# Optimization experiments

Hardware: AMD Instinct MI355X
Metric: run time of the kernel (lower is better)

## Reference

```python
import jax, jax.numpy as jnp
import numpy as np

N, DEG, F_IN, HID, OUT = 20000, 16, 128, 128, 64
E = N * DEG


def setup_inputs() -> dict:
    key = jax.random.key(0)
    ks = jax.random.split(key, 12)
    s = 0.05  # small init scale to keep activations stable
    x = jax.random.normal(ks[0], (N, F_IN), jnp.float32)
    # PyG LSTM aggregation requires edges sorted by destination; fixed degree DEG
    src = jax.random.randint(ks[1], (E,), 0, N, dtype=jnp.int32)
    dst = jnp.repeat(jnp.arange(N, dtype=jnp.int32), DEG)
    edge_index = jnp.stack([src, dst])  # [2, E]
    return {
        "x": x,
        "edge_index": edge_index,
        "lstm_Wih": jax.random.normal(ks[2], (4, 4 * HID, F_IN), jnp.float32) * s,
        "lstm_Whh": jax.random.normal(ks[3], (4, 4 * HID, HID), jnp.float32) * s,
        "lstm_bih": jax.random.normal(ks[4], (4, 4 * HID), jnp.float32) * s,
        "lstm_bhh": jax.random.normal(ks[5], (4, 4 * HID), jnp.float32) * s,
        "linl_W123": jax.random.normal(ks[6], (3, HID, HID), jnp.float32) * s,
        "linl_b123": jax.random.normal(ks[7], (3, HID), jnp.float32) * s,
        "linr_W123": jax.random.normal(ks[8], (3, HID, HID), jnp.float32) * s,
        "linl_W4": jax.random.normal(ks[9], (OUT, HID), jnp.float32) * s,
        "linl_b4": jax.random.normal(ks[10], (OUT,), jnp.float32) * s,
        "linr_W4": jax.random.normal(ks[11], (OUT, HID), jnp.float32) * s,
    }


def _lstm_last(msgs, Wih, Whh, bih, bhh):
    """Run an LSTM over the padded neighbor sequence, return h at last step.
    msgs: [n, deg, f]. Matches PyG LSTMAggregation (lstm(x)[0][:, -1])."""
    n = msgs.shape[0]
    H = Whh.shape[1]
    b = bih + bhh  # torch LSTM adds both biases

    def step(carry, xt):  # xt: [n, f]
        h, c = carry
        g = xt @ Wih.T + h @ Whh.T + b  # [n, 4H], gate order i,f,g,o
        i, f, gg, o = jnp.split(g, 4, axis=-1)
        c = jax.nn.sigmoid(f) * c + jax.nn.sigmoid(i) * jnp.tanh(gg)
        h = jax.nn.sigmoid(o) * jnp.tanh(c)
        return (h, c), None

    h0 = jnp.zeros((n, H), msgs.dtype)
    (h, _), _ = jax.lax.scan(step, (h0, h0), jnp.swapaxes(msgs, 0, 1))
    return h


def _sage_conv(x, src, Wih, Whh, bih, bhh, Wl, bl, Wr):
    """SAGEConv(aggr='lstm'): lin_l(lstm_agg(x_j)) + lin_r(x).
    Fixed degree + dst-sorted edges => to_dense_batch is a reshape."""
    n, f = x.shape
    msgs = x[src].reshape(n, DEG, f)  # gather neighbor (source) features
    agg = _lstm_last(msgs, Wih, Whh, bih, bhh)
    return agg @ Wl.T + bl + x @ Wr.T  # lin_r has no bias in PyG


def reference(x, edge_index, lstm_Wih, lstm_Whh, lstm_bih, lstm_bhh,
              linl_W123, linl_b123, linr_W123, linl_W4, linl_b4, linr_W4):
    src = edge_index[0]
    # eval mode: dropout is identity
    x1 = jax.nn.relu(_sage_conv(x, src, lstm_Wih[0], lstm_Whh[0], lstm_bih[0],
                                lstm_bhh[0], linl_W123[0], linl_b123[0], linr_W123[0]))
    x2 = jax.nn.relu(_sage_conv(x1, src, lstm_Wih[1], lstm_Whh[1], lstm_bih[1],
                                lstm_bhh[1], linl_W123[1], linl_b123[1], linr_W123[1]) + x1)
    x3 = jax.nn.relu(_sage_conv(x2, src, lstm_Wih[2], lstm_Whh[2], lstm_bih[2],
                                lstm_bhh[2], linl_W123[2], linl_b123[2], linr_W123[2]) + x2)
    x4 = _sage_conv(x3, src, lstm_Wih[3], lstm_Whh[3], lstm_bih[3], lstm_bhh[3],
                    linl_W4, linl_b4, linr_W4)
    return x4
```

## Files before the change

kernel.cpp:

```cpp
#include <hip/hip_runtime.h>


#define N_NODES 20000
#define DEG 16

typedef __bf16 bf16x8 __attribute__((ext_vector_type(8)));
typedef float f32x4 __attribute__((ext_vector_type(4)));

__device__ inline unsigned short f2bf(float f) {
  unsigned u = __builtin_bit_cast(unsigned, f);
  u += 0x7fffu + ((u >> 16) & 1u);
  return (unsigned short)(u >> 16);
}
__device__ inline float fexp2(float x) {
#if __has_builtin(__builtin_amdgcn_exp2f)
  return __builtin_amdgcn_exp2f(x);
#else
  return exp2f(x);
#endif
}
__device__ inline float frcp(float x) {
#if __has_builtin(__builtin_amdgcn_rcpf)
  return __builtin_amdgcn_rcpf(x);
#else
  return 1.f / x;
#endif
}
__device__ inline float sigm(float x) { return frcp(1.f + fexp2(-1.44269504f * x)); }
__device__ inline float tanh_(float x) { return frcp(1.f + fexp2(-2.88539008f * x)) * 2.f - 1.f; }

__device__ inline void barrier_lds() {
  asm volatile("s_waitcnt lgkmcnt(0)\n\ts_barrier" ::: "memory");
}

__global__ __launch_bounds__(256) void prep_weights(
    const float* __restrict__ Wih, const float* __restrict__ Whh,
    const float* __restrict__ bih, const float* __restrict__ bhh,
    unsigned short* __restrict__ WihB, unsigned short* __restrict__ WhhB,
    float* __restrict__ bsum) {
  int tid = blockIdx.x * 256 + threadIdx.x;
  float4 a = *(const float4*)(Wih + tid * 4);
  ushort4 o;
  o.x = f2bf(a.x); o.y = f2bf(a.y); o.z = f2bf(a.z); o.w = f2bf(a.w);
  *(ushort4*)(WihB + tid * 4) = o;
  float4 b = *(const float4*)(Whh + tid * 4);
  ushort4 p;
  p.x = f2bf(b.x); p.y = f2bf(b.y); p.z = f2bf(b.z); p.w = f2bf(b.w);
  *(ushort4*)(WhhB + tid * 4) = p;
  if (tid < 2048) bsum[tid] = bih[tid] + bhh[tid];
}

__global__ __launch_bounds__(256) void cast_bf(
    const float* __restrict__ x, unsigned short* __restrict__ xb) {
  int tid = blockIdx.x * 256 + threadIdx.x;
  float4 v = *(const float4*)(x + tid * 4);
  ushort4 o;
  o.x = f2bf(v.x); o.y = f2bf(v.y); o.z = f2bf(v.z); o.w = f2bf(v.w);
  *(ushort4*)(xb + tid * 4) = o;
}

__global__ __launch_bounds__(512, 2) void lstm_fused(
    const unsigned short* __restrict__ xbf,
    const int* __restrict__ src,
    const unsigned short* __restrict__ WihB,
    const unsigned short* __restrict__ WhhB,
    const float* __restrict__ bsum,
    float* __restrict__ agg) {
  __shared__ __align__(16) unsigned char xsb[2][32 * 256];
  __shared__ __align__(16) unsigned char hbuf[2][32 * 256];
  __shared__ __align__(16) int idx_s[512];
  const int tid = threadIdx.x;
  const int lane = tid & 63, w = tid >> 6;
  const int l15 = lane & 15, l4 = lane >> 4;
  const int node0 = blockIdx.x * 32;
  const int colb = w * 16 + l15;

  idx_s[(tid & 15) * 32 + (tid >> 4)] = src[node0 * DEG + tid];

  bf16x8 bwx[4][4], bwh[4][4];
  float bs[4];
#pragma unroll
  for (int g = 0; g < 4; ++g) {
#pragma unroll
    for (int kt = 0; kt < 4; ++kt) {
      bwx[g][kt] = *(const bf16x8*)(WihB + (g * 128 + colb) * 128 + kt * 32 + l4 * 8);
      bwh[g][kt] = *(const bf16x8*)(WhhB + (g * 128 + colb) * 128 + kt * 32 + l4 * 8);
    }
    bs[g] = bsum[g * 128 + colb];
  }
  barrier_lds();

  const int erow = w * 4 + l4;
  const int schunk = l15 ^ (erow & 7);

  {
    int idx = idx_s[erow];
    uint4 v = *(const uint4*)(xbf + idx * 128 + schunk * 8);
    *(uint4*)(&xsb[0][erow * 256 + l15 * 16]) = v;
  }
  barrier_lds();

  float c[2][4] = {{0.f, 0.f, 0.f, 0.f}, {0.f, 0.f, 0.f, 0.f}};

  for (int t = 0; t < 16; ++t) {
    uint4 xstg;
    if (t < 15) {
      int idx = idx_s[(t + 1) * 32 + erow];
      xstg = *(const uint4*)(xbf + idx * 128 + schunk * 8);
    }

    const unsigned char* xrb = xsb[t & 1];
    f32x4 acc[2][4];
#pragma unroll
    for (int rt = 0; rt < 2; ++rt)
#pragma unroll
      for (int g = 0; g < 4; ++g) acc[rt][g] = (f32x4){bs[g], bs[g], bs[g], bs[g]};

#pragma unroll
    for (int rt = 0; rt < 2; ++rt) {
      bf16x8 afx[4];
#pragma unroll
      for (int kt = 0; kt < 4; ++kt) {
        int m = rt * 16 + l15;
        int byte = (m * 256 + kt * 64 + l4 * 16) ^ ((m & 7) << 4);
        afx[kt] = *(const bf16x8*)(xrb + byte);
      }
#pragma unroll
      for (int g = 0; g < 4; ++g)
#pragma unroll
        for (int kt = 0; kt < 4; ++kt)
          acc[rt][g] = __builtin_amdgcn_mfma_f32_16x16x32_bf16(afx[kt], bwx[g][kt],
                                                               acc[rt][g], 0, 0, 0);
    }

    if (t > 0) {
      const unsigned char* hb = hbuf[(t - 1) & 1];
#pragma unroll
      for (int rt = 0; rt < 2; ++rt) {
        bf16x8 afh[4];
#pragma unroll
        for (int kt = 0; kt < 4; ++kt) {
          int m = rt * 16 + l15;
          int byte = (m * 256 + kt * 64 + l4 * 16) ^ ((m & 7) << 4);
          afh[kt] = *(const bf16x8*)(hb + byte);
        }
#pragma unroll
        for (int g = 0; g < 4; ++g)
#pragma unroll
          for (int kt = 0; kt < 4; ++kt)
            acc[rt][g] = __builtin_amdgcn_mfma_f32_16x16x32_bf16(afh[kt], bwh[g][kt],
                                                                 acc[rt][g], 0, 0, 0);
      }
    }

    float hn[2][4];
#pragma unroll
    for (int rt = 0; rt < 2; ++rt)
#pragma unroll
      for (int r = 0; r < 4; ++r) {
        float ig = sigm(acc[rt][0][r]), fg = sigm(acc[rt][1][r]);
        float gg = tanh_(acc[rt][2][r]), og = sigm(acc[rt][3][r]);
        float cn = fg * c[rt][r] + ig * gg;
        c[rt][r] = cn;
        hn[rt][r] = og * tanh_(cn);
      }

    if (t < 15) {
      unsigned char* hw = hbuf[t & 1];
#pragma unroll
      for (int rt = 0; rt < 2; ++rt)
#pragma unroll
        for (int r = 0; r < 4; ++r) {
          int m = rt * 16 + l4 * 4 + r;
          int byte = (m * 256 + colb * 2) ^ ((m & 7) << 4);
          *(__bf16*)(hw + byte) = (__bf16)hn[rt][r];
        }
      *(uint4*)(&xsb[(t + 1) & 1][erow * 256 + l15 * 16]) = xstg;
      barrier_lds();
    } else {
#pragma unroll
      for (int rt = 0; rt < 2; ++rt)
#pragma unroll
        for (int r = 0; r < 4; ++r)
          agg[(node0 + rt * 16 + l4 * 4 + r) * 128 + colb] = hn[rt][r];
    }
  }
}

__global__ __launch_bounds__(256) void gemm_out(
    const float* __restrict__ A1,
    const float* __restrict__ A2,
    const float* __restrict__ Wl, const float* __restrict__ bl,
    const float* __restrict__ Wr,
    const float* __restrict__ resid,
    float* __restrict__ out,
    unsigned short* __restrict__ outbf,
    int NOUT, int do_relu, int Nrows) {
  __shared__ __align__(16) unsigned char As[64 * 512];
  const int tid = threadIdx.x;
  const int lane = tid & 63, w = tid >> 6;
  const int l15 = lane & 15, l4 = lane >> 4;
  const int row0 = blockIdx.x * 64;

#pragma unroll
  for (int i = 0; i < 16; ++i) {
    int flat = i * 1024 + tid * 4;
    int r = flat >> 8, c = flat & 255;
    int grow = row0 + r;
    float4 v;
    if (grow < Nrows)
      v = (c < 128) ? *(const float4*)(A1 + grow * 128 + c)
                    : *(const float4*)(A2 + grow * 128 + (c - 128));
    else
      v = make_float4(0.f, 0.f, 0.f, 0.f);
    ushort4 b;
    b.x = f2bf(v.x); b.y = f2bf(v.y); b.z = f2bf(v.z); b.w = f2bf(v.w);
    int byte = (r * 512 + c * 2) ^ ((r & 7) << 4);
    *(ushort4*)(As + byte) = b;
  }
  __syncthreads();

  const int colg = blockIdx.y * 64 + w * 16 + l15;
  bf16x8 bw[8];
#pragma unroll
  for (int kt = 0; kt < 8; ++kt) {
    const float* bp = (kt < 4) ? (Wl + colg * 128 + kt * 32 + l4 * 8)
                               : (Wr + colg * 128 + (kt - 4) * 32 + l4 * 8);
    float4 a = *(const float4*)bp;
    float4 b = *(const float4*)(bp + 4);
    bf16x8 v;
    v[0] = (__bf16)a.x; v[1] = (__bf16)a.y; v[2] = (__bf16)a.z; v[3] = (__bf16)a.w;
    v[4] = (__bf16)b.x; v[5] = (__bf16)b.y; v[6] = (__bf16)b.z; v[7] = (__bf16)b.w;
    bw[kt] = v;
  }

  f32x4 acc[4];
#pragma unroll
  for (int rt = 0; rt < 4; ++rt) acc[rt] = (f32x4){0.f, 0.f, 0.f, 0.f};

#pragma unroll
  for (int kt = 0; kt < 8; ++kt) {
#pragma unroll
    for (int rt = 0; rt < 4; ++rt) {
      int m = rt * 16 + l15;
      int byte = (m * 512 + kt * 64 + l4 * 16) ^ ((m & 7) << 4);
      bf16x8 af = *(const bf16x8*)(As + byte);
      acc[rt] = __builtin_amdgcn_mfma_f32_16x16x32_bf16(af, bw[kt], acc[rt], 0, 0, 0);
    }
  }

  const float bias = bl[colg];
#pragma unroll
  for (int rt = 0; rt < 4; ++rt)
#pragma unroll
    for (int r = 0; r < 4; ++r) {
      int grow = row0 + rt * 16 + l4 * 4 + r;
      if (grow < Nrows) {
        float v = acc[rt][r] + bias;
        if (resid) v += resid[grow * 128 + colg];
        if (do_relu) v = fmaxf(v, 0.f);
        out[grow * NOUT + colg] = v;
        if (outbf) outbf[grow * 128 + colg] = f2bf(v);
      }
    }
}

extern "C" void kernel_launch(void* const* d_in, const int* in_sizes, int n_in,
                              void* d_out, int out_size, void* d_ws, size_t ws_size,
                              hipStream_t stream) {
  const float* X = (const float*)d_in[0];
  const int* src = (const int*)d_in[1];
  const float* Wih = (const float*)d_in[2];
  const float* Whh = (const float*)d_in[3];
  const float* bih = (const float*)d_in[4];
  const float* bhh = (const float*)d_in[5];
  const float* Wl123 = (const float*)d_in[6];
  const float* bl123 = (const float*)d_in[7];
  const float* Wr123 = (const float*)d_in[8];
  const float* Wl4 = (const float*)d_in[9];
  const float* bl4 = (const float*)d_in[10];
  const float* Wr4 = (const float*)d_in[11];
  float* out = (float*)d_out;

  char* ws = (char*)d_ws;
  unsigned short* xbf = (unsigned short*)ws;
  float* agg = (float*)(ws + 5120000);
  float* xb0 = (float*)(ws + 15360000);
  float* xb1 = (float*)(ws + 25600000);
  unsigned short* WihB = (unsigned short*)(ws + 35840000);
  unsigned short* WhhB = (unsigned short*)(ws + 36364288);
  float* bsumW = (float*)(ws + 36888576);

  prep_weights<<<dim3(256), 256, 0, stream>>>(Wih, Whh, bih, bhh, WihB, WhhB, bsumW);
  cast_bf<<<dim3(2500), 256, 0, stream>>>(X, xbf);

  const float* xcur = X;
  for (int L = 0; L < 4; ++L) {
    lstm_fused<<<dim3(625), 512, 0, stream>>>(xbf, src, WihB + L * 65536,
                                              WhhB + L * 65536, bsumW + L * 512, agg);
    if (L < 3) {
      float* nxt = (L & 1) ? xb1 : xb0;
      gemm_out<<<dim3(313, 2), 256, 0, stream>>>(agg, xcur, Wl123 + L * 16384,
                                                 bl123 + L * 128, Wr123 + L * 16384,
                                                 (L >= 1) ? xcur : nullptr, nxt, xbf,
                                                 128, 1, N_NODES);
      xcur = nxt;
    } else {
      gemm_out<<<dim3(313, 1), 256, 0, stream>>>(agg, xcur, Wl4, bl4, Wr4, nullptr, out,
                                                 nullptr, 64, 0, N_NODES);
    }
  }
}
```

Baseline: 546.0 us.

## Process 80 nodes per LSTM block and interleave per-row-tile gate compute

Each LSTM block now handles 80 nodes (5 row tiles) instead of 32, so the per-block weight register load is amortized over more nodes and the grid drops from 625 to 250 blocks. The loop is restructured so each row tile runs its x and h MFMAs, gate math and h store in sequence, which keeps only one tile's accumulators live and lets activation math overlap with the next tile's MFMAs. Gather staging grows to three uint4 loads per thread. The risks are that 250 blocks leaves many of the MI355X's CUs underused, and that the larger LDS footprint may reduce occupancy.

```diff
diff --git a/kernel.cpp b/kernel.cpp
--- a/kernel.cpp
+++ b/kernel.cpp
@@ -3,6 +3,8 @@
 
 #define N_NODES 20000
 #define DEG 16
+#define NPB 80
+#define RT 5
 
 typedef __bf16 bf16x8 __attribute__((ext_vector_type(8)));
 typedef float f32x4 __attribute__((ext_vector_type(4)));
@@ -66,16 +68,23 @@
     const unsigned short* __restrict__ WhhB,
     const float* __restrict__ bsum,
     float* __restrict__ agg) {
-  __shared__ __align__(16) unsigned char xsb[2][32 * 256];
-  __shared__ __align__(16) unsigned char hbuf[2][32 * 256];
-  __shared__ __align__(16) int idx_s[512];
+  __shared__ __align__(16) unsigned char xsb[2][NPB * 256];
+  __shared__ __align__(16) unsigned char hbuf[2][NPB * 256];
+  __shared__ __align__(16) int idx_s[NPB * DEG];
   const int tid = threadIdx.x;
   const int lane = tid & 63, w = tid >> 6;
   const int l15 = lane & 15, l4 = lane >> 4;
-  const int node0 = blockIdx.x * 32;
+  const int node0 = blockIdx.x * NPB;
   const int colb = w * 16 + l15;
 
-  idx_s[(tid & 15) * 32 + (tid >> 4)] = src[node0 * DEG + tid];
+#pragma unroll
+  for (int i = 0; i < 3; ++i) {
+    int task = tid + i * 512;
+    if (task < NPB * DEG) {
+      int node = task >> 4, t = task & 15;
+      idx_s[t * NPB + node] = src[node0 * DEG + task];
+    }
+  }
 
   bf16x8 bwx[4][4], bwh[4][4];
   float bs[4];
@@ -90,99 +99,95 @@
   }
   barrier_lds();
 
-  const int erow = w * 4 + l4;
-  const int schunk = l15 ^ (erow & 7);
+  const int task0 = tid, task1 = tid + 512;
+  const int row0s = task0 >> 4, ch0 = task0 & 15;
+  const int row1s = task1 >> 4, ch1 = task1 & 15;
+  const int task2 = tid + 1024;
+  const bool p2 = task2 < NPB * 16;
+  const int row2s = task2 >> 4, ch2 = task2 & 15;
 
   {
-    int idx = idx_s[erow];
-    uint4 v = *(const uint4*)(xbf + idx * 128 + schunk * 8);
-    *(uint4*)(&xsb[0][erow * 256 + l15 * 16]) = v;
+    uint4 v0 = *(const uint4*)(xbf + idx_s[row0s] * 128 + (ch0 ^ (row0s & 7)) * 8);
+    uint4 v1 = *(const uint4*)(xbf + idx_s[row1s] * 128 + (ch1 ^ (row1s & 7)) * 8);
+    *(uint4*)(&xsb[0][row0s * 256 + ch0 * 16]) = v0;
+    *(uint4*)(&xsb[0][row1s * 256 + ch1 * 16]) = v1;
+    if (p2) {
+      uint4 v2 = *(const uint4*)(xbf + idx_s[row2s] * 128 + (ch2 ^ (row2s & 7)) * 8);
+      *(uint4*)(&xsb[0][row2s * 256 + ch2 * 16]) = v2;
+    }
   }
   barrier_lds();
 
-  float c[2][4] = {{0.f, 0.f, 0.f, 0.f}, {0.f, 0.f, 0.f, 0.f}};
-
+  float c[RT][4];
+#pragma unroll
+  for (int rt = 0; rt < RT; ++rt)
+#pragma unroll
+    for (int r = 0; r < 4; ++r) c[rt][r] = 0.f;
+
+#pragma unroll 2
   for (int t = 0; t < 16; ++t) {
-    uint4 xstg;
+    uint4 xstg0, xstg1, xstg2;
     if (t < 15) {
-      int idx = idx_s[(t + 1) * 32 + erow];
-      xstg = *(const uint4*)(xbf + idx * 128 + schunk * 8);
+      const int tb = (t + 1) * NPB;
+      xstg0 = *(const uint4*)(xbf + idx_s[tb + row0s] * 128 + (ch0 ^ (row0s & 7)) * 8);
+      xstg1 = *(const uint4*)(xbf + idx_s[tb + row1s] * 128 + (ch1 ^ (row1s & 7)) * 8);
+      if (p2)
+        xstg2 = *(const uint4*)(xbf + idx_s[tb + row2s] * 128 + (ch2 ^ (row2s & 7)) * 8);
     }
 
     const unsigned char* xrb = xsb[t & 1];
-    f32x4 acc[2][4];
-#pragma unroll
-    for (int rt = 0; rt < 2; ++rt)
-#pragma unroll
-      for (int g = 0; g < 4; ++g) acc[rt][g] = (f32x4){bs[g], bs[g], bs[g], bs[g]};
-
-#pragma unroll
-    for (int rt = 0; rt < 2; ++rt) {
-      bf16x8 afx[4];
+    const unsigned char* hb = hbuf[(t + 1) & 1];
+    unsigned char* hw = hbuf[t & 1];
+
+#pragma unroll
+    for (int rt = 0; rt < RT; ++rt) {
+      f32x4 acc[4];
+#pragma unroll
+      for (int g = 0; g < 4; ++g) acc[g] = (f32x4){bs[g], bs[g], bs[g], bs[g]};
+
+      const int m = rt * 16 + l15;
 #pragma unroll
       for (int kt = 0; kt < 4; ++kt) {
-        int m = rt * 16 + l15;
         int byte = (m * 256 + kt * 64 + l4 * 16) ^ ((m & 7) << 4);
-        afx[kt] = *(const bf16x8*)(xrb + byte);
+        bf16x8 a = *(const bf16x8*)(xrb + byte);
+#pragma unroll
+        for (int g = 0; g < 4; ++g)
+          acc[g] = __builtin_amdgcn_mfma_f32_16x16x32_bf16(a, bwx[g][kt], acc[g], 0, 0, 0);
       }
-#pragma unroll
-      for (int g = 0; g < 4; ++g)
-#pragma unroll
-        for (int kt = 0; kt < 4; ++kt)
-          acc[rt][g] = __builtin_amdgcn_mfma_f32_16x16x32_bf16(afx[kt], bwx[g][kt],
-                                                               acc[rt][g], 0, 0, 0);
-    }
-
-    if (t > 0) {
-      const unsigned char* hb = hbuf[(t - 1) & 1];
-#pragma unroll
-      for (int rt = 0; rt < 2; ++rt) {
-        bf16x8 afh[4];
+      if (t > 0) {
 #pragma unroll
         for (int kt = 0; kt < 4; ++kt) {
-          int m = rt * 16 + l15;
           int byte = (m * 256 + kt * 64 + l4 * 16) ^ ((m & 7) << 4);
-          afh[kt] = *(const bf16x8*)(hb + byte);
+          bf16x8 a = *(const bf16x8*)(hb + byte);
+#pragma unroll
+          for (int g = 0; g < 4; ++g)
+            acc[g] = __builtin_amdgcn_mfma_f32_16x16x32_bf16(a, bwh[g][kt], acc[g], 0, 0, 0);
         }
-#pragma unroll
-        for (int g = 0; g < 4; ++g)
-#pragma unroll
-          for (int kt = 0; kt < 4; ++kt)
-            acc[rt][g] = __builtin_amdgcn_mfma_f32_16x16x32_bf16(afh[kt], bwh[g][kt],
-                                                                 acc[rt][g], 0, 0, 0);
       }
-    }
-
-    float hn[2][4];
-#pragma unroll
-    for (int rt = 0; rt < 2; ++rt)
+
 #pragma unroll
       for (int r = 0; r < 4; ++r) {
-        float ig = sigm(acc[rt][0][r]), fg = sigm(acc[rt][1][r]);
-        float gg = tanh_(acc[rt][2][r]), og = sigm(acc[rt][3][r]);
+        float ig = sigm(acc[0][r]), fg = sigm(acc[1][r]);
+        float gg = tanh_(acc[2][r]), og = sigm(acc[3][r]);
         float cn = fg * c[rt][r] + ig * gg;
         c[rt][r] = cn;
-        hn[rt][r] = og * tanh_(cn);
+        float hv = og * tanh_(cn);
+        int mm = rt * 16 + l4 * 4 + r;
+        if (t < 15) {
+          int byte = (mm * 256 + colb * 2) ^ ((mm & 7) << 4);
+          *(__bf16*)(hw + byte) = (__bf16)hv;
+        } else {
+          agg[(node0 + mm) * 128 + colb] = hv;
+        }
       }
+    }
 
     if (t < 15) {
-      unsigned char* hw = hbuf[t & 1];
-#pragma unroll
-      for (int rt = 0; rt < 2; ++rt)
-#pragma unroll
-        for (int r = 0; r < 4; ++r) {
-          int m = rt * 16 + l4 * 4 + r;
-          int byte = (m * 256 + colb * 2) ^ ((m & 7) << 4);
-          *(__bf16*)(hw + byte) = (__bf16)hn[rt][r];
-        }
-      *(uint4*)(&xsb[(t + 1) & 1][erow * 256 + l15 * 16]) = xstg;
+      unsigned char* xw = xsb[(t + 1) & 1];
+      *(uint4*)(&xw[row0s * 256 + ch0 * 16]) = xstg0;
+      *(uint4*)(&xw[row1s * 256 + ch1 * 16]) = xstg1;
+      if (p2) *(uint4*)(&xw[row2s * 256 + ch2 * 16]) = xstg2;
       barrier_lds();
-    } else {
-#pragma unroll
-      for (int rt = 0; rt < 2; ++rt)
-#pragma unroll
-        for (int r = 0; r < 4; ++r)
-          agg[(node0 + rt * 16 + l4 * 4 + r) * 128 + colb] = hn[rt][r];
     }
   }
 }
@@ -296,7 +301,7 @@
 
   const float* xcur = X;
   for (int L = 0; L < 4; ++L) {
-    lstm_fused<<<dim3(625), 512, 0, stream>>>(xbf, src, WihB + L * 65536,
+    lstm_fused<<<dim3(250), 512, 0, stream>>>(xbf, src, WihB + L * 65536,
                                               WhhB + L * 65536, bsumW + L * 512, agg);
     if (L < 3) {
       float* nxt = (L & 1) ? xb1 : xb0;
```

Result: faster. 467.9 us (-14.3%).
